# Kernel tuning notes

Hardware: AMD Instinct MI355X
Metric: run time of the kernel (lower is better)

## Reference

```python
import jax, jax.numpy as jnp
import numpy as np

B, T, F, H = 256, 128, 1024, 512  # batch, input_size (time window), feature_dim, hidden_size


def setup_inputs() -> dict:
    key = jax.random.key(0)
    ks = jax.random.split(key, 7)
    in1 = T + 2 * H
    return {
        "h": jax.random.normal(ks[0], (B, H), dtype=jnp.float32),
        "s": jax.random.normal(ks[1], (B, H), dtype=jnp.float32),
        "x": jax.random.normal(ks[2], (B, T, F), dtype=jnp.float32),
        "W1": jax.random.normal(ks[3], (T, in1), dtype=jnp.float32) / np.sqrt(in1),
        "b1": jnp.zeros((T,), dtype=jnp.float32),
        "W2": jax.random.normal(ks[4], (1, T), dtype=jnp.float32) / np.sqrt(T),
        "b2": jnp.zeros((1,), dtype=jnp.float32),
    }


def reference(h, s, x, W1, b1, W2, b2):
    feature_dim = x.shape[-1]
    xp = jnp.transpose(x, (2, 0, 1))                     # [F, B, T]
    hb = jnp.broadcast_to(h[None], (feature_dim,) + h.shape)  # [F, B, H]
    sb = jnp.broadcast_to(s[None], (feature_dim,) + s.shape)  # [F, B, H]
    cat = jnp.concatenate([xp, hb, sb], axis=-1)         # [F, B, T+2H]
    u = jnp.einsum('fbk,tk->fbt', cat, W1) + b1          # [F, B, T]
    e = jnp.einsum('fbt,ot->fbo', jnp.tanh(u), W2) + b2  # [F, B, 1]
    alpha = jax.nn.softmax(e, axis=0)[..., 0]            # softmax over feature dim -> [F, B]
    return alpha.T                                       # [B, F]
```

## Files before the change

kernel.cpp:

```cpp
#include <hip/hip_runtime.h>
#include <hip/hip_bf16.h>


#define B_N 256
#define T_N 128
#define F_N 1024
#define H_N 512
#define IN1 1152

typedef __bf16 bf16x8 __attribute__((ext_vector_type(8)));
typedef float f32x16 __attribute__((ext_vector_type(16)));
typedef float f32x4_t __attribute__((ext_vector_type(4)));
typedef unsigned int u32x4 __attribute__((ext_vector_type(4)));

__device__ __forceinline__ float wave_reduce_sum(float v) {
#pragma unroll
  for (int off = 32; off >= 1; off >>= 1) v += __shfl_xor(v, off, 64);
  return v;
}
__device__ __forceinline__ float wave_reduce_max(float v) {
#pragma unroll
  for (int off = 32; off >= 1; off >>= 1) v = fmaxf(v, __shfl_xor(v, off, 64));
  return v;
}
__device__ __forceinline__ float tanh_fast(float u) {
  u = fminf(fmaxf(u, -15.f), 15.f);
  float e2 = __expf(2.f * u);
  return (e2 - 1.f) / (e2 + 1.f);
}
__device__ __forceinline__ unsigned bfbits(float f) {
  return (unsigned)__builtin_bit_cast(unsigned short, (__bf16)f);
}
__device__ __forceinline__ float dot4(float4 a, float4 b) {
  return a.x * b.x + a.y * b.y + a.z * b.z + a.w * b.w;
}

__global__ __launch_bounds__(256) void kA_c(const float* __restrict__ h,
                                            const float* __restrict__ s,
                                            const float* __restrict__ W1,
                                            const float* __restrict__ b1,
                                            float* __restrict__ c) {
  int tid = threadIdx.x, lane = tid & 63, wave = tid >> 6;
  int t = blockIdx.x >> 1, bh = blockIdx.x & 1;
  const float4* wrow = reinterpret_cast<const float4*>(W1 + (size_t)t * IN1 + T_N);
  float4 w0 = wrow[lane], w1v = wrow[64 + lane], w2v = wrow[128 + lane], w3v = wrow[192 + lane];
  float b1t = b1[t];
  int b0 = bh * 128;
#pragma unroll 2
  for (int bi = 0; bi < 32; ++bi) {
    int b = b0 + wave + bi * 4;
    const float4* hr = reinterpret_cast<const float4*>(h + (size_t)b * H_N);
    const float4* sr = reinterpret_cast<const float4*>(s + (size_t)b * H_N);
    float acc = dot4(w0, hr[lane]) + dot4(w1v, hr[64 + lane]) +
                dot4(w2v, sr[lane]) + dot4(w3v, sr[64 + lane]);
    acc = wave_reduce_sum(acc);
    if (lane == 0) c[(size_t)b * T_N + t] = acc + b1t;
  }
}

__global__ __launch_bounds__(256) void kA_frag(const float* __restrict__ W1,
                                               unsigned short* __restrict__ w1frag) {
  int i = blockIdx.x * 256 + threadIdx.x;
  int p0 = i * 2;
  int j = p0 & 7;
  int lane = (p0 >> 3) & 63;
  int kk = (p0 >> 9) & 7;
  int tt = (p0 >> 12) & 3;
  int t = tt * 32 + (lane & 31);
  int k = kk * 16 + 8 * (lane >> 5) + j;
  const float2 w = *reinterpret_cast<const float2*>(W1 + t * IN1 + k);
  *reinterpret_cast<unsigned*>(w1frag + p0) = bfbits(w.x) | (bfbits(w.y) << 16);
}

__global__ __launch_bounds__(256) void kB_e(const float* __restrict__ x,
                                            const unsigned short* __restrict__ w1frag,
                                            const float* __restrict__ c,
                                            const float* __restrict__ W2,
                                            const float* __restrict__ b2,
                                            float* __restrict__ e) {
  __shared__ __align__(16) unsigned short w1lds[16384];
  __shared__ __align__(16) unsigned char xlds[32768];
  __shared__ __align__(16) float clds[T_N];
  __shared__ __align__(16) float w2lds[T_N];
  __shared__ __align__(16) float epart[4][T_N];
  int tid = threadIdx.x;
  int b = blockIdx.x >> 3;
  int fc = blockIdx.x & 7;
  const int fbase = fc * 128;

  {
    const uint4* src = reinterpret_cast<const uint4*>(w1frag);
    uint4* dst = reinterpret_cast<uint4*>(w1lds);
#pragma unroll
    for (int i = 0; i < 8; ++i) dst[tid + 256 * i] = src[tid + 256 * i];
  }
  {
    const float* xb = x + (size_t)b * T_N * F_N + fbase;
#pragma unroll
    for (int i = 0; i < 8; ++i) {
      int u = tid + 256 * i;
      int kq = u >> 6, fp = u & 63;
      const float* base = xb + (size_t)(kq * 4) * F_N + fp * 2;
      float2 r0 = *reinterpret_cast<const float2*>(base);
      float2 r1 = *reinterpret_cast<const float2*>(base + F_N);
      float2 r2 = *reinterpret_cast<const float2*>(base + 2 * F_N);
      float2 r3 = *reinterpret_cast<const float2*>(base + 3 * F_N);
      u32x4 pk;
      pk[0] = bfbits(r0.x) | (bfbits(r1.x) << 16);
      pk[1] = bfbits(r2.x) | (bfbits(r3.x) << 16);
      pk[2] = bfbits(r0.y) | (bfbits(r1.y) << 16);
      pk[3] = bfbits(r2.y) | (bfbits(r3.y) << 16);
      *reinterpret_cast<u32x4*>(xlds + kq * 1024 + fp * 16) = pk;
    }
  }
  if (tid < T_N) clds[tid] = c[(size_t)b * T_N + tid];
  else w2lds[tid - T_N] = W2[tid - T_N];
  __syncthreads();

  const int lane = tid & 63, wave = tid >> 6;
  const int g = lane >> 5, l31 = lane & 31;
  const bf16x8* af = reinterpret_cast<const bf16x8*>(w1lds);

  f32x16 acc0 = {}, acc1 = {}, acc2 = {}, acc3 = {};
#pragma unroll
  for (int kk = 0; kk < 8; ++kk) {
    bf16x8 afr = af[wave * 512 + kk * 64 + lane];
    const unsigned char* bbase = xlds + (kk * 4 + 2 * g) * 1024 + l31 * 8;
#define BFRAG(C)                                                                    \
  ({                                                                                \
    uint2 lo = *reinterpret_cast<const uint2*>(bbase + (C) * 256);                  \
    uint2 hi = *reinterpret_cast<const uint2*>(bbase + (C) * 256 + 1024);           \
    u32x4 q = {lo.x, lo.y, hi.x, hi.y};                                             \
    __builtin_bit_cast(bf16x8, q);                                                  \
  })
    acc0 = __builtin_amdgcn_mfma_f32_32x32x16_bf16(afr, BFRAG(0), acc0, 0, 0, 0);
    acc1 = __builtin_amdgcn_mfma_f32_32x32x16_bf16(afr, BFRAG(1), acc1, 0, 0, 0);
    acc2 = __builtin_amdgcn_mfma_f32_32x32x16_bf16(afr, BFRAG(2), acc2, 0, 0, 0);
    acc3 = __builtin_amdgcn_mfma_f32_32x32x16_bf16(afr, BFRAG(3), acc3, 0, 0, 0);
#undef BFRAG
  }

  const int tbase = wave * 32 + 4 * g;
  float es0 = 0.f, es1 = 0.f, es2 = 0.f, es3 = 0.f;
#pragma unroll
  for (int q = 0; q < 4; ++q) {
    f32x4_t cq = *reinterpret_cast<const f32x4_t*>(&clds[tbase + 8 * q]);
    f32x4_t wq = *reinterpret_cast<const f32x4_t*>(&w2lds[tbase + 8 * q]);
#pragma unroll
    for (int r = 0; r < 4; ++r) {
      int reg = q * 4 + r;
      es0 += wq[r] * tanh_fast(acc0[reg] + cq[r]);
      es1 += wq[r] * tanh_fast(acc1[reg] + cq[r]);
      es2 += wq[r] * tanh_fast(acc2[reg] + cq[r]);
      es3 += wq[r] * tanh_fast(acc3[reg] + cq[r]);
    }
  }
  es0 += __shfl_xor(es0, 32, 64);
  es1 += __shfl_xor(es1, 32, 64);
  es2 += __shfl_xor(es2, 32, 64);
  es3 += __shfl_xor(es3, 32, 64);
  if (g == 0) {
    epart[wave][l31] = es0;
    epart[wave][32 + l31] = es1;
    epart[wave][64 + l31] = es2;
    epart[wave][96 + l31] = es3;
  }
  __syncthreads();
  if (tid < T_N) {
    e[(size_t)b * F_N + fbase + tid] =
        epart[0][tid] + epart[1][tid] + epart[2][tid] + epart[3][tid] + b2[0];
  }
}

__global__ __launch_bounds__(256) void kC_softmax(float* __restrict__ out) {
  int b = blockIdx.x, tid = threadIdx.x;
  int lane = tid & 63, wid = tid >> 6;
  float* row = out + (size_t)b * F_N;
  float v[4];
#pragma unroll
  for (int q = 0; q < 4; ++q) v[q] = row[tid + 256 * q];
  float m = fmaxf(fmaxf(v[0], v[1]), fmaxf(v[2], v[3]));
  m = wave_reduce_max(m);
  __shared__ float rm[4], rs[4];
  if (lane == 0) rm[wid] = m;
  __syncthreads();
  float M = fmaxf(fmaxf(rm[0], rm[1]), fmaxf(rm[2], rm[3]));
  float ssum = 0.f;
#pragma unroll
  for (int q = 0; q < 4; ++q) {
    v[q] = __expf(v[q] - M);
    ssum += v[q];
  }
  ssum = wave_reduce_sum(ssum);
  if (lane == 0) rs[wid] = ssum;
  __syncthreads();
  float S = rs[0] + rs[1] + rs[2] + rs[3];
  float inv = 1.f / S;
#pragma unroll
  for (int q = 0; q < 4; ++q) row[tid + 256 * q] = v[q] * inv;
}

extern "C" void kernel_launch(void* const* d_in, const int* in_sizes, int n_in,
                              void* d_out, int out_size, void* d_ws, size_t ws_size,
                              hipStream_t stream) {
  const float* h = (const float*)d_in[0];
  const float* s = (const float*)d_in[1];
  const float* x = (const float*)d_in[2];
  const float* W1 = (const float*)d_in[3];
  const float* b1 = (const float*)d_in[4];
  const float* W2 = (const float*)d_in[5];
  const float* b2 = (const float*)d_in[6];
  float* out = (float*)d_out;

  float* c_ws = (float*)d_ws;
  unsigned short* w1frag = (unsigned short*)((char*)d_ws + B_N * T_N * 4);

  kA_c<<<256, 256, 0, stream>>>(h, s, W1, b1, c_ws);
  kA_frag<<<32, 256, 0, stream>>>(W1, w1frag);
  kB_e<<<2048, 256, 0, stream>>>(x, w1frag, c_ws, W2, b2, out);
  kC_softmax<<<256, 256, 0, stream>>>(out);
}
```

Measured before the change: 242.6 us.

## Read W1 fragments from global, widen x loads, split kA_c across more blocks

The main kernel no longer stages the 32KB bf16 W1 fragment array in LDS. Each wave now reads its A fragments straight from global memory (L2-resident), which halves LDS use per block and adds a launch-bounds hint for 4 blocks per SIMD-level occupancy. The x staging loop now uses float4 loads and writes two packed 16-byte chunks per thread, halving loop iterations, and the k-loop is only partly unrolled. The small c-computation kernel is split over 512 blocks instead of 256. The trade-off is global/L2 latency on the A-fragment loads in the MFMA loop against higher occupancy and less LDS fill traffic.

```diff
diff --git a/kernel.cpp b/kernel.cpp
--- a/kernel.cpp
+++ b/kernel.cpp
@@ -41,13 +41,13 @@
                                             const float* __restrict__ b1,
                                             float* __restrict__ c) {
   int tid = threadIdx.x, lane = tid & 63, wave = tid >> 6;
-  int t = blockIdx.x >> 1, bh = blockIdx.x & 1;
+  int t = blockIdx.x >> 2, bq = blockIdx.x & 3;
   const float4* wrow = reinterpret_cast<const float4*>(W1 + (size_t)t * IN1 + T_N);
   float4 w0 = wrow[lane], w1v = wrow[64 + lane], w2v = wrow[128 + lane], w3v = wrow[192 + lane];
   float b1t = b1[t];
-  int b0 = bh * 128;
+  int b0 = bq * 64;
 #pragma unroll 2
-  for (int bi = 0; bi < 32; ++bi) {
+  for (int bi = 0; bi < 16; ++bi) {
     int b = b0 + wave + bi * 4;
     const float4* hr = reinterpret_cast<const float4*>(h + (size_t)b * H_N);
     const float4* sr = reinterpret_cast<const float4*>(s + (size_t)b * H_N);
@@ -72,13 +72,12 @@
   *reinterpret_cast<unsigned*>(w1frag + p0) = bfbits(w.x) | (bfbits(w.y) << 16);
 }
 
-__global__ __launch_bounds__(256) void kB_e(const float* __restrict__ x,
-                                            const unsigned short* __restrict__ w1frag,
-                                            const float* __restrict__ c,
-                                            const float* __restrict__ W2,
-                                            const float* __restrict__ b2,
-                                            float* __restrict__ e) {
-  __shared__ __align__(16) unsigned short w1lds[16384];
+__global__ __launch_bounds__(256, 4) void kB_e(const float* __restrict__ x,
+                                               const unsigned short* __restrict__ w1frag,
+                                               const float* __restrict__ c,
+                                               const float* __restrict__ W2,
+                                               const float* __restrict__ b2,
+                                               float* __restrict__ e) {
   __shared__ __align__(16) unsigned char xlds[32768];
   __shared__ __align__(16) float clds[T_N];
   __shared__ __align__(16) float w2lds[T_N];
@@ -88,41 +87,42 @@
   int fc = blockIdx.x & 7;
   const int fbase = fc * 128;
 
-  {
-    const uint4* src = reinterpret_cast<const uint4*>(w1frag);
-    uint4* dst = reinterpret_cast<uint4*>(w1lds);
-#pragma unroll
-    for (int i = 0; i < 8; ++i) dst[tid + 256 * i] = src[tid + 256 * i];
-  }
+  if (tid < T_N) clds[tid] = c[(size_t)b * T_N + tid];
+  else w2lds[tid - T_N] = W2[tid - T_N];
+
   {
     const float* xb = x + (size_t)b * T_N * F_N + fbase;
 #pragma unroll
-    for (int i = 0; i < 8; ++i) {
+    for (int i = 0; i < 4; ++i) {
       int u = tid + 256 * i;
-      int kq = u >> 6, fp = u & 63;
-      const float* base = xb + (size_t)(kq * 4) * F_N + fp * 2;
-      float2 r0 = *reinterpret_cast<const float2*>(base);
-      float2 r1 = *reinterpret_cast<const float2*>(base + F_N);
-      float2 r2 = *reinterpret_cast<const float2*>(base + 2 * F_N);
-      float2 r3 = *reinterpret_cast<const float2*>(base + 3 * F_N);
-      u32x4 pk;
-      pk[0] = bfbits(r0.x) | (bfbits(r1.x) << 16);
-      pk[1] = bfbits(r2.x) | (bfbits(r3.x) << 16);
-      pk[2] = bfbits(r0.y) | (bfbits(r1.y) << 16);
-      pk[3] = bfbits(r2.y) | (bfbits(r3.y) << 16);
-      *reinterpret_cast<u32x4*>(xlds + kq * 1024 + fp * 16) = pk;
+      int kq = u >> 5, fq = u & 31;
+      const float* base = xb + (size_t)(kq * 4) * F_N + fq * 4;
+      float4 r0 = *reinterpret_cast<const float4*>(base);
+      float4 r1 = *reinterpret_cast<const float4*>(base + F_N);
+      float4 r2 = *reinterpret_cast<const float4*>(base + 2 * F_N);
+      float4 r3 = *reinterpret_cast<const float4*>(base + 3 * F_N);
+      u32x4 pa, pb;
+      pa[0] = bfbits(r0.x) | (bfbits(r1.x) << 16);
+      pa[1] = bfbits(r2.x) | (bfbits(r3.x) << 16);
+      pa[2] = bfbits(r0.y) | (bfbits(r1.y) << 16);
+      pa[3] = bfbits(r2.y) | (bfbits(r3.y) << 16);
+      pb[0] = bfbits(r0.z) | (bfbits(r1.z) << 16);
+      pb[1] = bfbits(r2.z) | (bfbits(r3.z) << 16);
+      pb[2] = bfbits(r0.w) | (bfbits(r1.w) << 16);
+      pb[3] = bfbits(r2.w) | (bfbits(r3.w) << 16);
+      unsigned char* dst = xlds + kq * 1024 + fq * 32;
+      *reinterpret_cast<u32x4*>(dst) = pa;
+      *reinterpret_cast<u32x4*>(dst + 16) = pb;
     }
   }
-  if (tid < T_N) clds[tid] = c[(size_t)b * T_N + tid];
-  else w2lds[tid - T_N] = W2[tid - T_N];
   __syncthreads();
 
   const int lane = tid & 63, wave = tid >> 6;
   const int g = lane >> 5, l31 = lane & 31;
-  const bf16x8* af = reinterpret_cast<const bf16x8*>(w1lds);
+  const bf16x8* af = reinterpret_cast<const bf16x8*>(w1frag);
 
   f32x16 acc0 = {}, acc1 = {}, acc2 = {}, acc3 = {};
-#pragma unroll
+#pragma unroll 4
   for (int kk = 0; kk < 8; ++kk) {
     bf16x8 afr = af[wave * 512 + kk * 64 + lane];
     const unsigned char* bbase = xlds + (kk * 4 + 2 * g) * 1024 + l31 * 8;
@@ -215,7 +215,7 @@
   float* c_ws = (float*)d_ws;
   unsigned short* w1frag = (unsigned short*)((char*)d_ws + B_N * T_N * 4);
 
-  kA_c<<<256, 256, 0, stream>>>(h, s, W1, b1, c_ws);
+  kA_c<<<512, 256, 0, stream>>>(h, s, W1, b1, c_ws);
   kA_frag<<<32, 256, 0, stream>>>(W1, w1frag);
   kB_e<<<2048, 256, 0, stream>>>(x, w1frag, c_ws, W2, b2, out);
   kC_softmax<<<256, 256, 0, stream>>>(out);
```

After: 233.4 us. 1.04x faster.
